# Performance work log

Measured on AMD Instinct MI355X. Metric: run time of the kernel, lower is better.

The kernel has to match this reference:

```python
import jax, jax.numpy as jnp
import numpy as np

NUM_VECTORS = 8192
LATENT_DIM = 256
BETA = 0.25


def setup_inputs() -> dict:
    key = jax.random.key(0)
    k1, k2 = jax.random.split(key)
    z = jax.random.normal(k1, (16, LATENT_DIM, 32, 32), dtype=jnp.float32)
    # nn.Embedding weight initialized uniform(-1/K, 1/K)
    emb_weight = jax.random.uniform(
        k2, (NUM_VECTORS, LATENT_DIM), dtype=jnp.float32,
        minval=-1.0 / NUM_VECTORS, maxval=1.0 / NUM_VECTORS)
    return {"z": z, "emb_weight": emb_weight}


def reference(z, emb_weight):
    # z: [B, C, H, W] -> [B, H, W, C]
    z_bhwc = jnp.transpose(z, (0, 2, 3, 1))
    B, H, W, C = z_bhwc.shape
    z_flat = z_bhwc.reshape(-1, C)  # [N, C]

    # Squared distances: ||z||^2 + ||e||^2 - 2 z.e  -> [N, K]
    d = (jnp.sum(z_flat ** 2, axis=1, keepdims=True)
         + jnp.sum(emb_weight ** 2, axis=1)
         - 2.0 * jnp.einsum('nc,kc->nk', z_flat, emb_weight))
    idx = jnp.argmin(d, axis=1)  # [N]

    z_q = emb_weight[idx].reshape(B, H, W, C)

    sg = jax.lax.stop_gradient
    loss = (jnp.mean((sg(z_q) - z_bhwc) ** 2)
            + BETA * jnp.mean((z_q - sg(z_bhwc)) ** 2))

    # Straight-through estimator
    z_q_st = z_bhwc + sg(z_q - z_bhwc)
    z_q_out = jnp.transpose(z_q_st, (0, 3, 1, 2))  # [B, C, H, W]
    return z_q_out, idx, loss
```

## Files before the change

### kernel.cpp

```cpp
#include <hip/hip_runtime.h>
#include <math.h>

#define NB   16
#define CC   256
#define NPTS 16384
#define KK   8192
#define Z_OUT 4194304

#define WS_ENORM 16448
#define WS_CCNT  24640
#define WS_CIDX  41024
#define CAND_CAP 64
#define LCAP     96
#define MARGIN   4.0e-4f

typedef short v8s __attribute__((ext_vector_type(8)));
typedef float v4f __attribute__((ext_vector_type(4)));

__device__ __forceinline__ void gl_lds16(const void* g, void* l) {
    __builtin_amdgcn_global_load_lds((const __attribute__((address_space(1))) void*)g,
                                     (__attribute__((address_space(3))) void*)l, 16, 0, 0);
}
__device__ __forceinline__ unsigned short f2bf(float f) {
    unsigned int u = __float_as_uint(f);
    return (unsigned short)((u + 0x7FFFu + ((u >> 16) & 1u)) >> 16);
}
__device__ __forceinline__ unsigned fenc(float f) {
    unsigned u = __float_as_uint(f);
    return (u & 0x80000000u) ? ~u : (u | 0x80000000u);
}
__device__ __forceinline__ float fdec(unsigned m) {
    unsigned u = (m & 0x80000000u) ? (m & 0x7fffffffu) : ~m;
    return __uint_as_float(u);
}

__global__ void k_prep_z(const float* __restrict__ z, unsigned short* __restrict__ zb16) {
    __shared__ float ts[64][65];
    const int hw0 = blockIdx.x * 64, c0 = blockIdx.y * 64, b = blockIdx.z;
    const int tid = threadIdx.x;
#pragma unroll
    for (int p = 0; p < 4; ++p) {
        int u = p * 256 + tid;
        int ci = u >> 4, j4 = (u & 15) << 2;
        float4 v = *(const float4*)(z + (size_t)b * 262144 + (size_t)(c0 + ci) * 1024 + hw0 + j4);
        ts[ci][j4 + 0] = v.x; ts[ci][j4 + 1] = v.y; ts[ci][j4 + 2] = v.z; ts[ci][j4 + 3] = v.w;
    }
    __syncthreads();
#pragma unroll
    for (int p = 0; p < 4; ++p) {
        int u = p * 256 + tid;
        int hj = u >> 4, i4 = (u & 15) << 2;
        ushort4 o = make_ushort4(f2bf(ts[i4 + 0][hj]), f2bf(ts[i4 + 1][hj]),
                                 f2bf(ts[i4 + 2][hj]), f2bf(ts[i4 + 3][hj]));
        *(ushort4*)(zb16 + (size_t)(b * 1024 + hw0 + hj) * 256 + c0 + i4) = o;
    }
}

__global__ void k_prep_e(const float* __restrict__ emb, unsigned short* __restrict__ ebf,
                         float* __restrict__ enorm, float* __restrict__ lossAcc,
                         int* __restrict__ doneCnt) {
    const int w = threadIdx.x >> 6, lane = threadIdx.x & 63;
    const int k = blockIdx.x * 4 + w;
    const int i = k * CC + lane * 4;
    float4 v = *(const float4*)(emb + i);
    *(ushort4*)(ebf + i) = make_ushort4(f2bf(v.x), f2bf(v.y), f2bf(v.z), f2bf(v.w));
    float s = v.x * v.x + v.y * v.y + v.z * v.z + v.w * v.w;
    for (int off = 32; off > 0; off >>= 1) s += __shfl_down(s, off);
    if (lane == 0) enorm[k] = s;
    if (blockIdx.x == 0 && threadIdx.x == 0) { lossAcc[0] = 0.0f; doneCnt[0] = 0; }
}

__global__ __launch_bounds__(512, 2)
void k_cand(const unsigned short* __restrict__ zb16, const unsigned short* __restrict__ ebf,
            int* __restrict__ candCnt, int* __restrict__ candI) {
    __shared__ short    Bs[8][4][512];
    __shared__ unsigned runmaxU[64];
    __shared__ int      cnt[64];
    __shared__ int      lstK[64][LCAP];
    __shared__ float    lstD[64][LCAP];

    const int tid  = threadIdx.x;
    const int lane = tid & 63;
    const int w    = tid >> 6;
    const int nb   = blockIdx.x << 6;
    const int m16  = lane & 15, q = lane >> 4;

    if (tid < 64) { runmaxU[tid] = 0x007FFFFFu;  cnt[tid] = 0; }

#pragma unroll
    for (int p = 0; p < 4; ++p) {
        const int g8 = p * 8 + w;
        const int cc = g8 >> 2, nt = g8 & 3;
        const unsigned short* g = zb16 + (size_t)(nb + nt * 16 + m16) * 256 + cc * 32 + q * 8;
        gl_lds16(g, &Bs[cc][nt][lane * 8]);
    }

    auto loadA = [&](v8s (&a)[4], int kbr, int cc) {
#pragma unroll
        for (int kt = 0; kt < 4; ++kt)
            a[kt] = *(const v8s*)(ebf + (size_t)(kbr + (kt << 4) + m16) * 256 + (cc << 5) + q * 8);
    };
    auto loadB = [&](v8s (&b)[4], int cc) {
#pragma unroll
        for (int nt = 0; nt < 4; ++nt) b[nt] = *(const v8s*)&Bs[cc][nt][lane * 8];
    };

    v8s aR[4][4];
    v8s bP[4], bN[4];

    const int kb0 = w << 6;
    loadA(aR[0], kb0, 0);
    loadA(aR[1], kb0, 1);
    loadA(aR[2], kb0, 2);
    __syncthreads();
    loadB(bP, 0);

#pragma unroll 1
    for (int s = 0; s < 16; ++s) {
        const int kb  = ((s << 3) + w) << 6;
        const int kbn = (s < 15) ? kb + 512 : kb;
        v4f acc[16];
#pragma unroll
        for (int i = 0; i < 16; ++i) acc[i] = (v4f){0.f, 0.f, 0.f, 0.f};

#pragma unroll
        for (int cc = 0; cc < 8; ++cc) {
            if ((cc & 1) == 0) loadB(bN, (cc + 1) & 7);
            else               loadB(bP, (cc + 1) & 7);
            {
                const int tcc = cc + 3;
                if (tcc < 8) loadA(aR[tcc & 3], kb,  tcc);
                else         loadA(aR[tcc & 3], kbn, tcc - 8);
            }
#pragma unroll
            for (int kt = 0; kt < 4; ++kt)
#pragma unroll
                for (int nt = 0; nt < 4; ++nt)
                    acc[kt * 4 + nt] = __builtin_amdgcn_mfma_f32_16x16x32_bf16(
                        aR[cc & 3][kt], ((cc & 1) ? bN[nt] : bP[nt]),
                        acc[kt * 4 + nt], 0, 0, 0);
        }

        float mx[4];
#pragma unroll
        for (int nt = 0; nt < 4; ++nt) {
            float m = acc[0 * 4 + nt][0];
#pragma unroll
            for (int kt = 0; kt < 4; ++kt)
#pragma unroll
                for (int r = 0; r < 4; ++r) m = fmaxf(m, acc[kt * 4 + nt][r]);
            m = fmaxf(m, __shfl_xor(m, 16));
            m = fmaxf(m, __shfl_xor(m, 32));
            mx[nt] = m;
            if (lane < 16) atomicMax(&runmaxU[nt * 16 + lane], fenc(m));
        }
#pragma unroll
        for (int nt = 0; nt < 4; ++nt) {
            const int nl = nt * 16 + m16;
            const float thr = fmaxf(fdec(runmaxU[nl]), mx[nt]) - MARGIN;
#pragma unroll
            for (int kt = 0; kt < 4; ++kt)
#pragma unroll
                for (int r = 0; r < 4; ++r) {
                    if (acc[kt * 4 + nt][r] >= thr) {
                        int k = kb + (kt << 4) + q * 4 + r;
                        int pos = atomicAdd(&cnt[nl], 1);
                        if (pos < LCAP) { lstK[nl][pos] = k; lstD[nl][pos] = acc[kt * 4 + nt][r]; }
                    }
                }
        }
        if (s == 3 || s == 9) __syncthreads();
    }

    __syncthreads();
    if (tid < 64) {
        const int n = nb + tid;
        const int c = cnt[tid];
        if (c > LCAP) {
            candCnt[n] = KK;
        } else {
            const float thr = fdec(runmaxU[tid]) - MARGIN;
            int kept = 0;
            for (int i = 0; i < c; ++i) {
                if (lstD[tid][i] >= thr) {
                    if (kept < CAND_CAP) candI[(size_t)n * CAND_CAP + kept] = lstK[tid][i];
                    ++kept;
                }
            }
            candCnt[n] = (kept > CAND_CAP) ? KK : kept;
        }
    }
}

__global__ __launch_bounds__(256)
void k_final(const float* __restrict__ z, const float* __restrict__ emb,
             const float* __restrict__ enorm, const int* __restrict__ candCnt,
             const int* __restrict__ candI, float* __restrict__ out,
             float* __restrict__ idxf, float* __restrict__ lossAcc,
             int* __restrict__ doneCnt, float* __restrict__ outLoss) {
    __shared__ float zl[32][261];
    __shared__ int   kis[32];
    __shared__ float red[256];
    const int bid = blockIdx.x;
    const int b = bid >> 5, hw0 = (bid & 31) << 5;
    const int tid = threadIdx.x;
    const int lane = tid & 63, w = tid >> 6;

#pragma unroll
    for (int p = 0; p < 8; ++p) {
        const int u = p * 256 + tid;
        const int c = u >> 3, j4 = (u & 7) << 2;
        float4 v = *(const float4*)(z + (size_t)b * 262144 + (size_t)c * 1024 + hw0 + j4);
        zl[j4 + 0][c] = v.x; zl[j4 + 1][c] = v.y; zl[j4 + 2][c] = v.z; zl[j4 + 3][c] = v.w;
    }
    __syncthreads();

#pragma unroll 1
    for (int rr = 0; rr < 8; ++rr) {
        const int j = w * 8 + rr;
        const int n = b * 1024 + hw0 + j;
        const float4 zv = *(const float4*)&zl[j][lane * 4];
        float zn = zv.x * zv.x;
        zn = fmaf(zv.y, zv.y, zn); zn = fmaf(zv.z, zv.z, zn); zn = fmaf(zv.w, zv.w, zn);
#pragma unroll
        for (int off = 1; off < 64; off <<= 1) zn += __shfl_xor(zn, off);
        const int cnt = candCnt[n];
        float bd = __builtin_inff();
        int   bk = 0x7fffffff;
        if (cnt <= CAND_CAP) {
#pragma unroll 1
            for (int i = 0; i < cnt; ++i) {
                const int k = candI[(size_t)n * CAND_CAP + i];
                const float4 ev = *(const float4*)(emb + (size_t)k * CC + lane * 4);
                float p = zv.x * ev.x;
                p = fmaf(zv.y, ev.y, p);
                p = fmaf(zv.z, ev.z, p);
                p = fmaf(zv.w, ev.w, p);
#pragma unroll
                for (int off = 1; off < 64; off <<= 1) p += __shfl_xor(p, off);
                const float d = (zn + enorm[k]) - (p + p);
                if (d < bd || (d == bd && k < bk)) { bd = d; bk = k; }
            }
        } else {
#pragma unroll 1
            for (int k = 0; k < KK; ++k) {
                const float4 ev = *(const float4*)(emb + (size_t)k * CC + lane * 4);
                float p = zv.x * ev.x;
                p = fmaf(zv.y, ev.y, p);
                p = fmaf(zv.z, ev.z, p);
                p = fmaf(zv.w, ev.w, p);
#pragma unroll
                for (int off = 1; off < 64; off <<= 1) p += __shfl_xor(p, off);
                const float d = (zn + enorm[k]) - (p + p);
                if (d < bd) { bd = d; bk = k; }
            }
        }
        if (lane == 0) { idxf[n] = (float)bk; kis[j] = bk; }
    }
    __syncthreads();

    const int j  = tid & 31;
    const int cg = tid >> 5;
    const int ki0 = kis[j];
    const float* ep = emb + (size_t)ki0 * CC;
    float ls = 0.0f;
#pragma unroll 4
    for (int c = cg * 32; c < cg * 32 + 32; ++c) {
        float e  = ep[c];
        float zv = zl[j][c];
        out[(size_t)b * 262144 + (size_t)c * 1024 + hw0 + j] = e;
        float df = e - zv;
        ls = fmaf(df, df, ls);
    }
    red[tid] = ls;
    __syncthreads();
    for (int s2 = 128; s2 > 0; s2 >>= 1) {
        if (tid < s2) red[tid] += red[tid + s2];
        __syncthreads();
    }
    if (tid == 0) {
        atomicAdd(lossAcc, red[0]);
        __threadfence();
        int old = atomicAdd(doneCnt, 1);
        if (old == (int)gridDim.x - 1) {
            float tot = atomicAdd(lossAcc, 0.0f);
            float m = tot * (1.0f / 4194304.0f);
            outLoss[0] = m + 0.25f * m;
        }
    }
}

extern "C" void kernel_launch(void* const* d_in, const int* in_sizes, int n_in,
                              void* d_out, int out_size, void* d_ws, size_t ws_size,
                              hipStream_t stream) {
    const float* z   = (const float*)d_in[0];
    const float* emb = (const float*)d_in[1];
    float* outf = (float*)d_out;
    float* wsf  = (float*)d_ws;

    float* lossAcc = wsf;
    int*   doneCnt = (int*)(wsf + 1);
    float* enorm   = wsf + WS_ENORM;
    int*   candCnt = (int*)(wsf + WS_CCNT);
    int*   candI   = (int*)(wsf + WS_CIDX);

    unsigned short* zb16 = (unsigned short*)outf;
    unsigned short* ebf  = (unsigned short*)(outf + 2097152);

    k_prep_e<<<2048, 256, 0, stream>>>(emb, ebf, enorm, lossAcc, doneCnt);
    k_prep_z<<<dim3(16, 4, 16), 256, 0, stream>>>(z, zb16);
    k_cand<<<256, 512, 0, stream>>>(zb16, ebf, candCnt, candI);
    k_final<<<512, 256, 0, stream>>>(z, emb, enorm, candCnt, candI,
                                     outf, outf + Z_OUT, lossAcc, doneCnt,
                                     outf + Z_OUT + NPTS);
}
```

Measured before the change: 267.1 us.

## Merge prep kernels, halve final-kernel tile, prefetch candidate rows

Combines the embedding and z preprocessing kernels into one launch that branches on block index, removing one kernel launch. The final rescoring kernel now handles 16 points per block instead of 32, doubling the grid to 1024 blocks for better occupancy. Candidate indices are loaded once per wavefront and broadcast with shuffles, and the next embedding row is loaded one step ahead to hide global-load latency. The trade-off is more blocks each doing less work, with more register pressure from the prefetch.

```diff
diff --git a/kernel.cpp b/kernel.cpp
--- a/kernel.cpp
+++ b/kernel.cpp
@@ -34,40 +34,43 @@
     return __uint_as_float(u);
 }
 
-__global__ void k_prep_z(const float* __restrict__ z, unsigned short* __restrict__ zb16) {
-    __shared__ float ts[64][65];
-    const int hw0 = blockIdx.x * 64, c0 = blockIdx.y * 64, b = blockIdx.z;
+__global__ void k_prep(const float* __restrict__ z, const float* __restrict__ emb,
+                       unsigned short* __restrict__ zb16, unsigned short* __restrict__ ebf,
+                       float* __restrict__ enorm, float* __restrict__ lossAcc,
+                       int* __restrict__ doneCnt) {
+    const int bid = blockIdx.x;
     const int tid = threadIdx.x;
-#pragma unroll
-    for (int p = 0; p < 4; ++p) {
-        int u = p * 256 + tid;
-        int ci = u >> 4, j4 = (u & 15) << 2;
-        float4 v = *(const float4*)(z + (size_t)b * 262144 + (size_t)(c0 + ci) * 1024 + hw0 + j4);
-        ts[ci][j4 + 0] = v.x; ts[ci][j4 + 1] = v.y; ts[ci][j4 + 2] = v.z; ts[ci][j4 + 3] = v.w;
-    }
-    __syncthreads();
-#pragma unroll
-    for (int p = 0; p < 4; ++p) {
-        int u = p * 256 + tid;
-        int hj = u >> 4, i4 = (u & 15) << 2;
-        ushort4 o = make_ushort4(f2bf(ts[i4 + 0][hj]), f2bf(ts[i4 + 1][hj]),
-                                 f2bf(ts[i4 + 2][hj]), f2bf(ts[i4 + 3][hj]));
-        *(ushort4*)(zb16 + (size_t)(b * 1024 + hw0 + hj) * 256 + c0 + i4) = o;
-    }
-}
-
-__global__ void k_prep_e(const float* __restrict__ emb, unsigned short* __restrict__ ebf,
-                         float* __restrict__ enorm, float* __restrict__ lossAcc,
-                         int* __restrict__ doneCnt) {
-    const int w = threadIdx.x >> 6, lane = threadIdx.x & 63;
-    const int k = blockIdx.x * 4 + w;
-    const int i = k * CC + lane * 4;
-    float4 v = *(const float4*)(emb + i);
-    *(ushort4*)(ebf + i) = make_ushort4(f2bf(v.x), f2bf(v.y), f2bf(v.z), f2bf(v.w));
-    float s = v.x * v.x + v.y * v.y + v.z * v.z + v.w * v.w;
-    for (int off = 32; off > 0; off >>= 1) s += __shfl_down(s, off);
-    if (lane == 0) enorm[k] = s;
-    if (blockIdx.x == 0 && threadIdx.x == 0) { lossAcc[0] = 0.0f; doneCnt[0] = 0; }
+    if (bid < 2048) {
+        const int w = tid >> 6, lane = tid & 63;
+        const int k = bid * 4 + w;
+        const int i = k * CC + lane * 4;
+        float4 v = *(const float4*)(emb + i);
+        *(ushort4*)(ebf + i) = make_ushort4(f2bf(v.x), f2bf(v.y), f2bf(v.z), f2bf(v.w));
+        float s = v.x * v.x + v.y * v.y + v.z * v.z + v.w * v.w;
+        for (int off = 32; off > 0; off >>= 1) s += __shfl_down(s, off);
+        if (lane == 0) enorm[k] = s;
+        if (bid == 0 && tid == 0) { lossAcc[0] = 0.0f; doneCnt[0] = 0; }
+    } else {
+        __shared__ float ts[64][65];
+        const int b2 = bid - 2048;
+        const int hw0 = (b2 & 15) * 64, c0 = ((b2 >> 4) & 3) * 64, b = b2 >> 6;
+#pragma unroll
+        for (int p = 0; p < 4; ++p) {
+            int u = p * 256 + tid;
+            int ci = u >> 4, j4 = (u & 15) << 2;
+            float4 v = *(const float4*)(z + (size_t)b * 262144 + (size_t)(c0 + ci) * 1024 + hw0 + j4);
+            ts[ci][j4 + 0] = v.x; ts[ci][j4 + 1] = v.y; ts[ci][j4 + 2] = v.z; ts[ci][j4 + 3] = v.w;
+        }
+        __syncthreads();
+#pragma unroll
+        for (int p = 0; p < 4; ++p) {
+            int u = p * 256 + tid;
+            int hj = u >> 4, i4 = (u & 15) << 2;
+            ushort4 o = make_ushort4(f2bf(ts[i4 + 0][hj]), f2bf(ts[i4 + 1][hj]),
+                                     f2bf(ts[i4 + 2][hj]), f2bf(ts[i4 + 3][hj]));
+            *(ushort4*)(zb16 + (size_t)(b * 1024 + hw0 + hj) * 256 + c0 + i4) = o;
+        }
+    }
 }
 
 __global__ __launch_bounds__(512, 2)
@@ -198,26 +201,26 @@
              const int* __restrict__ candI, float* __restrict__ out,
              float* __restrict__ idxf, float* __restrict__ lossAcc,
              int* __restrict__ doneCnt, float* __restrict__ outLoss) {
-    __shared__ float zl[32][261];
-    __shared__ int   kis[32];
+    __shared__ float zl[16][261];
+    __shared__ int   kis[16];
     __shared__ float red[256];
     const int bid = blockIdx.x;
-    const int b = bid >> 5, hw0 = (bid & 31) << 5;
+    const int b = bid >> 6, hw0 = (bid & 63) << 4;
     const int tid = threadIdx.x;
     const int lane = tid & 63, w = tid >> 6;
 
 #pragma unroll
-    for (int p = 0; p < 8; ++p) {
+    for (int p = 0; p < 4; ++p) {
         const int u = p * 256 + tid;
-        const int c = u >> 3, j4 = (u & 7) << 2;
+        const int c = u >> 2, j4 = (u & 3) << 2;
         float4 v = *(const float4*)(z + (size_t)b * 262144 + (size_t)c * 1024 + hw0 + j4);
         zl[j4 + 0][c] = v.x; zl[j4 + 1][c] = v.y; zl[j4 + 2][c] = v.z; zl[j4 + 3][c] = v.w;
     }
     __syncthreads();
 
 #pragma unroll 1
-    for (int rr = 0; rr < 8; ++rr) {
-        const int j = w * 8 + rr;
+    for (int rr = 0; rr < 4; ++rr) {
+        const int j = w * 4 + rr;
         const int n = b * 1024 + hw0 + j;
         const float4 zv = *(const float4*)&zl[j][lane * 4];
         float zn = zv.x * zv.x;
@@ -228,18 +231,28 @@
         float bd = __builtin_inff();
         int   bk = 0x7fffffff;
         if (cnt <= CAND_CAP) {
+            int myk = 0;
+            if (lane < cnt) myk = candI[(size_t)n * CAND_CAP + lane];
+            if (cnt > 0) {
+                int kc = __shfl(myk, 0);
+                float4 ev = *(const float4*)(emb + (size_t)kc * CC + lane * 4);
 #pragma unroll 1
-            for (int i = 0; i < cnt; ++i) {
-                const int k = candI[(size_t)n * CAND_CAP + i];
-                const float4 ev = *(const float4*)(emb + (size_t)k * CC + lane * 4);
-                float p = zv.x * ev.x;
-                p = fmaf(zv.y, ev.y, p);
-                p = fmaf(zv.z, ev.z, p);
-                p = fmaf(zv.w, ev.w, p);
-#pragma unroll
-                for (int off = 1; off < 64; off <<= 1) p += __shfl_xor(p, off);
-                const float d = (zn + enorm[k]) - (p + p);
-                if (d < bd || (d == bd && k < bk)) { bd = d; bk = k; }
+                for (int i = 0; i < cnt; ++i) {
+                    const float4 evc = ev;
+                    const int kcur = kc;
+                    if (i + 1 < cnt) {
+                        kc = __shfl(myk, i + 1);
+                        ev = *(const float4*)(emb + (size_t)kc * CC + lane * 4);
+                    }
+                    float p = zv.x * evc.x;
+                    p = fmaf(zv.y, evc.y, p);
+                    p = fmaf(zv.z, evc.z, p);
+                    p = fmaf(zv.w, evc.w, p);
+#pragma unroll
+                    for (int off = 1; off < 64; off <<= 1) p += __shfl_xor(p, off);
+                    const float d = (zn + enorm[kcur]) - (p + p);
+                    if (d < bd || (d == bd && kcur < bk)) { bd = d; bk = kcur; }
+                }
             }
         } else {
 #pragma unroll 1
@@ -259,13 +272,13 @@
     }
     __syncthreads();
 
-    const int j  = tid & 31;
-    const int cg = tid >> 5;
+    const int j  = tid & 15;
+    const int cg = tid >> 4;
     const int ki0 = kis[j];
     const float* ep = emb + (size_t)ki0 * CC;
     float ls = 0.0f;
 #pragma unroll 4
-    for (int c = cg * 32; c < cg * 32 + 32; ++c) {
+    for (int c = cg * 16; c < cg * 16 + 16; ++c) {
         float e  = ep[c];
         float zv = zl[j][c];
         out[(size_t)b * 262144 + (size_t)c * 1024 + hw0 + j] = e;
@@ -307,10 +320,9 @@
     unsigned short* zb16 = (unsigned short*)outf;
     unsigned short* ebf  = (unsigned short*)(outf + 2097152);
 
-    k_prep_e<<<2048, 256, 0, stream>>>(emb, ebf, enorm, lossAcc, doneCnt);
-    k_prep_z<<<dim3(16, 4, 16), 256, 0, stream>>>(z, zb16);
+    k_prep<<<3072, 256, 0, stream>>>(z, emb, zb16, ebf, enorm, lossAcc, doneCnt);
     k_cand<<<256, 512, 0, stream>>>(zb16, ebf, candCnt, candI);
-    k_final<<<512, 256, 0, stream>>>(z, emb, enorm, candCnt, candI,
-                                     outf, outf + Z_OUT, lossAcc, doneCnt,
-                                     outf + Z_OUT + NPTS);
-}
+    k_final<<<1024, 256, 0, stream>>>(z, emb, enorm, candCnt, candI,
+                                      outf, outf + Z_OUT, lossAcc, doneCnt,
+                                      outf + Z_OUT + NPTS);
+}
```

Result: no change. 268.5 us (+0.6%).
